# Kernel optimization log

Measured on AMD Instinct MI355X. Metric: run time of the kernel, lower is better.

Reference implementation:

```python
import jax, jax.numpy as jnp
import numpy as np

N, E, F_IN, HID, NUM_CLASSES = 10000, 160000, 512, 1024, 100
NEG_SLOPE = 0.2  # PyG GATv2Conv default negative_slope


def setup_inputs() -> dict:
    key = jax.random.key(0)
    ks = jax.random.split(key, 10)
    return {
        "x": jax.random.normal(ks[0], (N, F_IN), jnp.float32),
        "edge_index": jax.random.randint(ks[1], (2, E), 0, N, dtype=jnp.int64)
        if jax.config.jax_enable_x64 else jax.random.randint(ks[1], (2, E), 0, N, dtype=jnp.int32),
        # GATv2Conv params (single head, out=1024): lin_l (source), lin_r (target), attention vector a, output bias
        "Wl": jax.random.normal(ks[2], (F_IN, HID), jnp.float32) / np.sqrt(F_IN),
        "bl": jnp.zeros((HID,), jnp.float32),
        "Wr": jax.random.normal(ks[3], (F_IN, HID), jnp.float32) / np.sqrt(F_IN),
        "br": jnp.zeros((HID,), jnp.float32),
        "att": jax.random.normal(ks[4], (HID,), jnp.float32) / np.sqrt(HID),
        "conv_b": jnp.zeros((HID,), jnp.float32),
        # MLP head: 1024 -> 512 -> 128 -> num_classes
        "W1": jax.random.normal(ks[5], (HID, 512), jnp.float32) / np.sqrt(HID),
        "b1": jnp.zeros((512,), jnp.float32),
        "W2": jax.random.normal(ks[6], (512, 128), jnp.float32) / np.sqrt(512),
        "b2": jnp.zeros((128,), jnp.float32),
        "Wc": jax.random.normal(ks[7], (128, NUM_CLASSES), jnp.float32) / np.sqrt(128),
        "bc": jnp.zeros((NUM_CLASSES,), jnp.float32),
    }


def _gatv2_conv(x, edge_index, Wl, bl, Wr, br, att, conv_b):
    """GATv2Conv, heads=1, add_self_loops=True, share_weights=False."""
    n = x.shape[0]
    loops = jnp.arange(n, dtype=edge_index.dtype)
    src = jnp.concatenate([edge_index[0], loops])  # message sources j
    dst = jnp.concatenate([edge_index[1], loops])  # message targets i
    xl = x @ Wl + bl  # [N, HID] source transform
    xr = x @ Wr + br  # [N, HID] target transform
    # e_ij = a^T LeakyReLU(xl_j + xr_i), per edge
    e = jax.nn.leaky_relu(xl[src] + xr[dst], negative_slope=NEG_SLOPE) @ att  # [E+N]
    # segment softmax over incoming edges of each target node (self-loops guarantee non-empty segments)
    m = jax.ops.segment_max(e, dst, num_segments=n)
    w = jnp.exp(e - m[dst])
    s = jax.ops.segment_sum(w, dst, num_segments=n)
    alpha = w / s[dst]  # [E+N]
    out = jax.ops.segment_sum(alpha[:, None] * xl[src], dst, num_segments=n)  # [N, HID]
    return out + conv_b


def reference(x, edge_index, Wl, bl, Wr, br, att, conv_b, W1, b1, W2, b2, Wc, bc):
    h = jax.nn.relu(_gatv2_conv(x, edge_index, Wl, bl, Wr, br, att, conv_b))
    h = jax.nn.relu(h @ W1 + b1)
    h = jax.nn.relu(h @ W2 + b2)
    return h @ Wc + bc
```

## Files before the change

### kernel.cpp

```cpp
#include <hip/hip_runtime.h>
#include <hip/hip_bf16.h>

constexpr int N_NODES = 10000;
constexpr int E_EDGES = 160000;
constexpr int F_IN    = 512;
constexpr int HID     = 1024;
constexpr int NCLS    = 100;
constexpr float NEG_SLOPE = 0.2f;

constexpr int BM = 128, BN = 128, BK = 32;
constexpr int M_PAD = ((N_NODES + BM - 1) / BM) * BM;
constexpr int DEG_CAP = 64;

typedef __attribute__((ext_vector_type(8))) short bf16x8;
typedef __attribute__((ext_vector_type(4))) float f32x4;

__device__ inline void load_lds_16(const void* g, void* l) {
    __builtin_amdgcn_global_load_lds(
        (const __attribute__((address_space(1))) void*)g,
        (__attribute__((address_space(3))) void*)l, 16, 0, 0);
}

__device__ inline float bf2f(short s) {
    unsigned u = ((unsigned)(unsigned short)s) << 16;
    return __builtin_bit_cast(float, u);
}

__device__ inline float rfl(float x) {
    return __builtin_bit_cast(float,
        __builtin_amdgcn_readfirstlane(__builtin_bit_cast(int, x)));
}

__device__ inline short4 cvt4(const f32x4 v, const float4 b, int relu) {
    float r0 = v[0] + b.x, r1 = v[1] + b.y, r2 = v[2] + b.z, r3 = v[3] + b.w;
    if (relu) {
        r0 = fmaxf(r0, 0.f); r1 = fmaxf(r1, 0.f);
        r2 = fmaxf(r2, 0.f); r3 = fmaxf(r3, 0.f);
    }
    short4 o;
    o.x = __builtin_bit_cast(short, __float2bfloat16(r0));
    o.y = __builtin_bit_cast(short, __float2bfloat16(r1));
    o.z = __builtin_bit_cast(short, __float2bfloat16(r2));
    o.w = __builtin_bit_cast(short, __float2bfloat16(r3));
    return o;
}

__global__ __launch_bounds__(256, 4) void gemm_mfma(
    const __hip_bfloat16* __restrict__ A, const __hip_bfloat16* __restrict__ Bt,
    const float* __restrict__ bias, int M, int K, int relu, int n_valid,
    __hip_bfloat16* __restrict__ Cb, int ldb)
{
    __shared__ __align__(16) short As[2][BM * BK];
    __shared__ __align__(16) short Bs[2][BN * BK];

    const int tid  = threadIdx.x;
    const int lane = tid & 63;
    const int w    = tid >> 6;
    const int m0   = blockIdx.y * BM;
    const int n0   = blockIdx.x * BN;

    f32x4 acc[4][4] = {};

    const int c0 = tid, c1 = tid + 256;
    const int r0 = c0 >> 2, cc0 = (c0 & 3) ^ ((r0 >> 2) & 3);
    const int r1 = c1 >> 2, cc1 = (c1 & 3) ^ ((r1 >> 2) & 3);

    const short* Ag0 = (const short*)A + (size_t)(m0 + r0) * K + cc0 * 8;
    const short* Ag1 = (const short*)A + (size_t)(m0 + r1) * K + cc1 * 8;
    const short* Bg0 = (const short*)Bt + (size_t)(n0 + r0) * K + cc0 * 8;
    const short* Bg1 = (const short*)Bt + (size_t)(n0 + r1) * K + cc1 * 8;

    const int wm = (w >> 1) * 64;
    const int wn = (w & 1) * 64;
    const int q  = lane >> 4;
    const int mr = lane & 15;
    const int sl = (q ^ (mr >> 2)) * 8;

    load_lds_16(Ag0, As[0] + c0 * 8);
    load_lds_16(Ag1, As[0] + c1 * 8);
    load_lds_16(Bg0, Bs[0] + c0 * 8);
    load_lds_16(Bg1, Bs[0] + c1 * 8);

    int cur = 0;
    for (int k0 = 0; k0 < K; k0 += BK) {
        __syncthreads();
        const int nxt = cur ^ 1;
        const int kn = k0 + BK;
        if (kn < K) {
            load_lds_16(Ag0 + kn, As[nxt] + c0 * 8);
            load_lds_16(Ag1 + kn, As[nxt] + c1 * 8);
            load_lds_16(Bg0 + kn, Bs[nxt] + c0 * 8);
            load_lds_16(Bg1 + kn, Bs[nxt] + c1 * 8);
        }

        bf16x8 af[4], bf[4];
        #pragma unroll
        for (int mt = 0; mt < 4; ++mt)
            af[mt] = *(const bf16x8*)&As[cur][(wm + mt * 16 + mr) * BK + sl];
        #pragma unroll
        for (int nt = 0; nt < 4; ++nt)
            bf[nt] = *(const bf16x8*)&Bs[cur][(wn + nt * 16 + mr) * BK + sl];
        #pragma unroll
        for (int mt = 0; mt < 4; ++mt)
            #pragma unroll
            for (int nt = 0; nt < 4; ++nt)
                acc[mt][nt] = __builtin_amdgcn_mfma_f32_16x16x32_bf16(
                    bf[nt], af[mt], acc[mt][nt], 0, 0, 0);
        cur = nxt;
    }

    #pragma unroll
    for (int mt = 0; mt < 4; ++mt) {
        const int gm = m0 + wm + mt * 16 + mr;
        if (gm >= M) continue;
        #pragma unroll
        for (int nt = 0; nt < 4; ++nt) {
            const int gn = n0 + wn + nt * 16 + q * 4;
            if (gn >= n_valid) continue;
            const float4 bv = *(const float4*)&bias[gn];
            short4 o = cvt4(acc[mt][nt], bv, relu);
            *(short4*)((short*)Cb + (size_t)gm * ldb + gn) = o;
        }
    }
}

__global__ __launch_bounds__(256, 4) void gemm_mfma_64(
    const __hip_bfloat16* __restrict__ A, const __hip_bfloat16* __restrict__ Bt,
    const float* __restrict__ bias, int M, int K, int relu, int n_valid,
    __hip_bfloat16* __restrict__ Cb, int ldb)
{
    __shared__ __align__(16) short As[2][64 * BK];
    __shared__ __align__(16) short Bs[2][BN * BK];

    const int tid  = threadIdx.x;
    const int lane = tid & 63;
    const int w    = tid >> 6;
    const int m0   = blockIdx.y * 64;
    const int n0   = blockIdx.x * BN;

    f32x4 acc[4][2] = {};

    const int ca = tid;
    const int ra = ca >> 2, cca = (ca & 3) ^ ((ra >> 2) & 3);
    const int c0 = tid, c1 = tid + 256;
    const int r0 = c0 >> 2, cc0 = (c0 & 3) ^ ((r0 >> 2) & 3);
    const int r1 = c1 >> 2, cc1 = (c1 & 3) ^ ((r1 >> 2) & 3);

    const short* Ag  = (const short*)A + (size_t)(m0 + ra) * K + cca * 8;
    const short* Bg0 = (const short*)Bt + (size_t)(n0 + r0) * K + cc0 * 8;
    const short* Bg1 = (const short*)Bt + (size_t)(n0 + r1) * K + cc1 * 8;

    const int wn = w * 32;
    const int q  = lane >> 4;
    const int mr = lane & 15;
    const int sl = (q ^ (mr >> 2)) * 8;

    load_lds_16(Ag,  As[0] + ca * 8);
    load_lds_16(Bg0, Bs[0] + c0 * 8);
    load_lds_16(Bg1, Bs[0] + c1 * 8);

    int cur = 0;
    for (int k0 = 0; k0 < K; k0 += BK) {
        __syncthreads();
        const int nxt = cur ^ 1;
        const int kn = k0 + BK;
        if (kn < K) {
            load_lds_16(Ag + kn,  As[nxt] + ca * 8);
            load_lds_16(Bg0 + kn, Bs[nxt] + c0 * 8);
            load_lds_16(Bg1 + kn, Bs[nxt] + c1 * 8);
        }

        bf16x8 af[4], bf[2];
        #pragma unroll
        for (int mt = 0; mt < 4; ++mt)
            af[mt] = *(const bf16x8*)&As[cur][(mt * 16 + mr) * BK + sl];
        #pragma unroll
        for (int nt = 0; nt < 2; ++nt)
            bf[nt] = *(const bf16x8*)&Bs[cur][(wn + nt * 16 + mr) * BK + sl];
        #pragma unroll
        for (int mt = 0; mt < 4; ++mt)
            #pragma unroll
            for (int nt = 0; nt < 2; ++nt)
                acc[mt][nt] = __builtin_amdgcn_mfma_f32_16x16x32_bf16(
                    bf[nt], af[mt], acc[mt][nt], 0, 0, 0);
        cur = nxt;
    }

    #pragma unroll
    for (int mt = 0; mt < 4; ++mt) {
        const int gm = m0 + mt * 16 + mr;
        if (gm >= M) continue;
        #pragma unroll
        for (int nt = 0; nt < 2; ++nt) {
            const int gn = n0 + wn + nt * 16 + q * 4;
            if (gn >= n_valid) continue;
            const float4 bv = *(const float4*)&bias[gn];
            short4 o = cvt4(acc[mt][nt], bv, relu);
            *(short4*)((short*)Cb + (size_t)gm * ldb + gn) = o;
        }
    }
}

constexpr int HS_LD = 136;

__global__ __launch_bounds__(256) void mlp_tail(
    const __hip_bfloat16* __restrict__ h1, const __hip_bfloat16* __restrict__ W2t,
    const float* __restrict__ b2, const __hip_bfloat16* __restrict__ Wct,
    const float* __restrict__ bc, float* __restrict__ out)
{
    __shared__ __align__(16) short As[2][BM * BK];
    __shared__ __align__(16) short Bs[2][BN * BK];
    __shared__ __align__(16) short Hs[128 * HS_LD];

    const int tid  = threadIdx.x;
    const int lane = tid & 63;
    const int w    = tid >> 6;
    const int m0   = blockIdx.x * BM;

    const int c0 = tid, c1 = tid + 256;
    const int r0 = c0 >> 2, cc0 = (c0 & 3) ^ ((r0 >> 2) & 3);
    const int r1 = c1 >> 2, cc1 = (c1 & 3) ^ ((r1 >> 2) & 3);

    const int wm = (w >> 1) * 64;
    const int wn = (w & 1) * 64;
    const int q  = lane >> 4;
    const int mr = lane & 15;
    const int sl = (q ^ (mr >> 2)) * 8;

    {
        f32x4 acc[4][4] = {};
        const short* Ag0 = (const short*)h1 + (size_t)(m0 + r0) * 512 + cc0 * 8;
        const short* Ag1 = (const short*)h1 + (size_t)(m0 + r1) * 512 + cc1 * 8;
        const short* Bg0 = (const short*)W2t + (size_t)r0 * 512 + cc0 * 8;
        const short* Bg1 = (const short*)W2t + (size_t)r1 * 512 + cc1 * 8;

        load_lds_16(Ag0, As[0] + c0 * 8);
        load_lds_16(Ag1, As[0] + c1 * 8);
        load_lds_16(Bg0, Bs[0] + c0 * 8);
        load_lds_16(Bg1, Bs[0] + c1 * 8);

        int cur = 0;
        for (int k0 = 0; k0 < 512; k0 += BK) {
            __syncthreads();
            const int nxt = cur ^ 1;
            const int kn = k0 + BK;
            if (kn < 512) {
                load_lds_16(Ag0 + kn, As[nxt] + c0 * 8);
                load_lds_16(Ag1 + kn, As[nxt] + c1 * 8);
                load_lds_16(Bg0 + kn, Bs[nxt] + c0 * 8);
                load_lds_16(Bg1 + kn, Bs[nxt] + c1 * 8);
            }
            bf16x8 af[4], bf[4];
            #pragma unroll
            for (int mt = 0; mt < 4; ++mt)
                af[mt] = *(const bf16x8*)&As[cur][(wm + mt * 16 + mr) * BK + sl];
            #pragma unroll
            for (int nt = 0; nt < 4; ++nt)
                bf[nt] = *(const bf16x8*)&Bs[cur][(wn + nt * 16 + mr) * BK + sl];
            #pragma unroll
            for (int mt = 0; mt < 4; ++mt)
                #pragma unroll
                for (int nt = 0; nt < 4; ++nt)
                    acc[mt][nt] = __builtin_amdgcn_mfma_f32_16x16x32_bf16(
                        bf[nt], af[mt], acc[mt][nt], 0, 0, 0);
            cur = nxt;
        }
        __syncthreads();
        #pragma unroll
        for (int mt = 0; mt < 4; ++mt) {
            const int ml = wm + mt * 16 + mr;
            #pragma unroll
            for (int nt = 0; nt < 4; ++nt) {
                const int nl = wn + nt * 16 + q * 4;
                const float4 bv = *(const float4*)&b2[nl];
                short4 o = cvt4(acc[mt][nt], bv, 1);
                *(short4*)&Hs[ml * HS_LD + nl] = o;
            }
        }
    }

    {
        f32x4 acc[4][4] = {};
        const short* Bg0 = (const short*)Wct + (size_t)r0 * 128 + cc0 * 8;
        const short* Bg1 = (const short*)Wct + (size_t)r1 * 128 + cc1 * 8;

        for (int k0 = 0; k0 < 128; k0 += BK) {
            __syncthreads();
            load_lds_16(Bg0 + k0, Bs[0] + c0 * 8);
            load_lds_16(Bg1 + k0, Bs[0] + c1 * 8);
            __syncthreads();

            bf16x8 af[4], bf[4];
            #pragma unroll
            for (int mt = 0; mt < 4; ++mt)
                af[mt] = *(const bf16x8*)&Hs[(wm + mt * 16 + mr) * HS_LD + k0 + q * 8];
            #pragma unroll
            for (int nt = 0; nt < 4; ++nt)
                bf[nt] = *(const bf16x8*)&Bs[0][(wn + nt * 16 + mr) * BK + sl];
            #pragma unroll
            for (int mt = 0; mt < 4; ++mt)
                #pragma unroll
                for (int nt = 0; nt < 4; ++nt)
                    acc[mt][nt] = __builtin_amdgcn_mfma_f32_16x16x32_bf16(
                        bf[nt], af[mt], acc[mt][nt], 0, 0, 0);
        }
        #pragma unroll
        for (int mt = 0; mt < 4; ++mt) {
            const int gm = m0 + wm + mt * 16 + mr;
            if (gm >= N_NODES) continue;
            #pragma unroll
            for (int nt = 0; nt < 4; ++nt) {
                const int gn = wn + nt * 16 + q * 4;
                if (gn >= NCLS) continue;
                const float4 bv = *(const float4*)&bc[gn];
                float4 o;
                o.x = acc[mt][nt][0] + bv.x;
                o.y = acc[mt][nt][1] + bv.y;
                o.z = acc[mt][nt][2] + bv.z;
                o.w = acc[mt][nt][3] + bv.w;
                *(float4*)(out + (size_t)gm * NCLS + gn) = o;
            }
        }
    }
}

__device__ void transpose_tile(const float* __restrict__ W,
                               __hip_bfloat16* __restrict__ Wt,
                               int K, int N, int NP, int bx, int by,
                               int tx, int ty, float (*t)[33])
{
    int n0 = bx * 32, k0 = by * 32;
    #pragma unroll
    for (int i = 0; i < 32; i += 8) {
        int k = k0 + ty + i, n = n0 + tx;
        t[ty + i][tx] = (k < K && n < N) ? W[(size_t)k * N + n] : 0.f;
    }
    __syncthreads();
    #pragma unroll
    for (int i = 0; i < 32; i += 8) {
        int n = n0 + ty + i, k = k0 + tx;
        if (n < NP && k < K)
            Wt[(size_t)n * K + k] = __float2bfloat16(t[tx][ty + i]);
    }
}

constexpr int PK_X    = M_PAD * F_IN / 1024;
constexpr int PK_WL   = PK_X + 512;
constexpr int PK_WR   = PK_WL + 512;
constexpr int PK_W1   = PK_WR + 512;
constexpr int PK_W2   = PK_W1 + 64;
constexpr int PK_WC   = PK_W2 + 16;
constexpr int PK_BLR  = PK_WC + 8;
constexpr int PK_EDGE = PK_BLR + (E_EDGES + 255) / 256;

__global__ __launch_bounds__(256) void pack_all(
    const float* __restrict__ x, __hip_bfloat16* __restrict__ xb,
    const float* __restrict__ Wl, const float* __restrict__ Wr,
    __hip_bfloat16* __restrict__ Wlrt,
    const float* __restrict__ W1, __hip_bfloat16* __restrict__ W1t,
    const float* __restrict__ W2, __hip_bfloat16* __restrict__ W2t,
    const float* __restrict__ Wc, __hip_bfloat16* __restrict__ Wct,
    const float* __restrict__ bl, const float* __restrict__ br,
    float* __restrict__ blr,
    const int* __restrict__ ei, int* __restrict__ cnt, int* __restrict__ srcs)
{
    __shared__ float t[32][33];
    const int b = blockIdx.x;
    const int tid = threadIdx.x;
    const int tx = tid & 31, ty = tid >> 5;

    if (b < PK_X) {
        int i = b * 256 + tid;
        int row = i >> 7;
        int base = i << 2;
        short4 o;
        if (row < N_NODES) {
            const float4 v = *(const float4*)(x + base);
            o.x = __builtin_bit_cast(short, __float2bfloat16(v.x));
            o.y = __builtin_bit_cast(short, __float2bfloat16(v.y));
            o.z = __builtin_bit_cast(short, __float2bfloat16(v.z));
            o.w = __builtin_bit_cast(short, __float2bfloat16(v.w));
        } else {
            o.x = o.y = o.z = o.w = 0;
        }
        *(short4*)((short*)xb + base) = o;
    } else if (b < PK_WL) {
        int l = b - PK_X;
        transpose_tile(Wl, Wlrt, F_IN, HID, HID, l & 31, l >> 5, tx, ty, t);
    } else if (b < PK_WR) {
        int l = b - PK_WL;
        transpose_tile(Wr, Wlrt + (size_t)HID * F_IN, F_IN, HID, HID,
                       l & 31, l >> 5, tx, ty, t);
    } else if (b < PK_W1) {
        int l = b - PK_WR;
        transpose_tile(W1, W1t, HID, 512, 512, l & 15, l >> 4, tx, ty, t);
    } else if (b < PK_W2) {
        int l = b - PK_W1;
        transpose_tile(W2, W2t, 512, 128, 128, l & 3, l >> 2, tx, ty, t);
    } else if (b < PK_WC) {
        int l = b - PK_W2;
        transpose_tile(Wc, Wct, 128, NCLS, 128, l & 3, l >> 2, tx, ty, t);
    } else if (b < PK_BLR) {
        int i = (b - PK_WC) * 256 + tid;
        if (i < HID) blr[i] = bl[i];
        else if (i < 2 * HID) blr[i] = br[i - HID];
    } else {
        int e = (b - PK_BLR) * 256 + tid;
        if (e < E_EDGES) {
            int s = ei[e], d = ei[E_EDGES + e];
            int r = atomicAdd(&cnt[d], 1);
            if (r < DEG_CAP) srcs[(size_t)d * DEG_CAP + r] = s;
        }
    }
}

__global__ __launch_bounds__(256) void gat_node(
    const __hip_bfloat16* __restrict__ xlr, const float* __restrict__ att,
    const float* __restrict__ conv_b,
    const int* __restrict__ cnt, const int* __restrict__ srcs,
    __hip_bfloat16* __restrict__ h)
{
    const int tid  = threadIdx.x;
    const int lane = tid & 63;
    const int wave = tid >> 6;
    const int nloc = wave >> 1;
    const int wsub = wave & 1;
    const int i    = blockIdx.x * 2 + nloc;

    __shared__ float O_s[2][16 * 64];
    __shared__ float ml_s[2][2];

    int deg = __builtin_amdgcn_readfirstlane(cnt[i]);
    if (deg > DEG_CAP) deg = DEG_CAP;
    const int total = deg + 1;
    const int last  = total - 1;
    const int* slist = srcs + (size_t)i * DEG_CAP;
    const short* base = (const short*)xlr;

    float xr_v[16], att_v[16];
    {
        const short* xri = base + (size_t)i * 2048 + HID + lane * 16;
        bf16x8 a0 = *(const bf16x8*)xri;
        bf16x8 a1 = *(const bf16x8*)(xri + 8);
        const float* ai = att + lane * 16;
        #pragma unroll
        for (int j = 0; j < 8; ++j) {
            xr_v[j] = bf2f(a0[j]);
            xr_v[8 + j] = bf2f(a1[j]);
        }
        #pragma unroll
        for (int j = 0; j < 16; ++j) att_v[j] = ai[j];
    }

    float m_w = -3e38f, l_w = 0.f;
    float O[16];
    #pragma unroll
    for (int j = 0; j < 16; ++j) O[j] = 0.f;

    int pos = wsub;
    if (pos < total) {
        int sc = __builtin_amdgcn_readfirstlane(pos < deg ? slist[pos] : i);
        int pn = (pos + 2 <= last) ? pos + 2 : last;
        int sn = __builtin_amdgcn_readfirstlane(pn < deg ? slist[pn] : i);
        const short* rp = base + (size_t)sc * 2048 + lane * 16;
        bf16x8 a0 = *(const bf16x8*)rp;
        bf16x8 a1 = *(const bf16x8*)(rp + 8);

        for (; pos < total; pos += 2) {
            const short* np = base + (size_t)sn * 2048 + lane * 16;
            bf16x8 b0 = *(const bf16x8*)np;
            bf16x8 b1 = *(const bf16x8*)(np + 8);
            int p2i = (pos + 4 <= last) ? pos + 4 : last;
            int s2 = p2i < deg ? slist[p2i] : i;

            float xf[16];
            #pragma unroll
            for (int j = 0; j < 8; ++j) {
                xf[j] = bf2f(a0[j]);
                xf[8 + j] = bf2f(a1[j]);
            }

            float p = 0.f;
            #pragma unroll
            for (int j = 0; j < 16; ++j) {
                float a = xf[j] + xr_v[j];
                a = fmaxf(a, NEG_SLOPE * a);
                p = __builtin_fmaf(att_v[j], a, p);
            }
            #pragma unroll
            for (int s = 1; s < 64; s <<= 1) p += __shfl_xor(p, s, 64);
            p = rfl(p);

            if (p > m_w) {
                const float scale = __expf(m_w - p);
                l_w = l_w * scale + 1.f;
                #pragma unroll
                for (int j = 0; j < 16; ++j) O[j] = O[j] * scale + xf[j];
                m_w = p;
            } else {
                const float alpha = __expf(p - m_w);
                l_w += alpha;
                #pragma unroll
                for (int j = 0; j < 16; ++j)
                    O[j] = __builtin_fmaf(alpha, xf[j], O[j]);
            }

            a0 = b0; a1 = b1;
            sn = __builtin_amdgcn_readfirstlane(s2);
        }
    }

    if (wsub == 1) {
        #pragma unroll
        for (int j = 0; j < 16; ++j) O_s[nloc][j * 64 + lane] = O[j];
        if (lane == 0) { ml_s[nloc][0] = m_w; ml_s[nloc][1] = l_w; }
    }
    __syncthreads();

    if (wsub == 0) {
        const float m1 = ml_s[nloc][0], l1 = ml_s[nloc][1];
        const float M  = fmaxf(m_w, m1);
        const float c0 = __expf(m_w - M);
        const float c1 = __expf(m1 - M);
        const float invL = 1.f / (l_w * c0 + l1 * c1);
        const float* cb = conv_b + lane * 16;
        bf16x8 o0, o1;
        #pragma unroll
        for (int j = 0; j < 8; ++j) {
            float r0 = __builtin_fmaf(
                c0 * O[j] + c1 * O_s[nloc][j * 64 + lane], invL, cb[j]);
            float r1 = __builtin_fmaf(
                c0 * O[8 + j] + c1 * O_s[nloc][(8 + j) * 64 + lane], invL,
                cb[8 + j]);
            r0 = fmaxf(r0, 0.f);
            r1 = fmaxf(r1, 0.f);
            o0[j] = __builtin_bit_cast(short, __float2bfloat16(r0));
            o1[j] = __builtin_bit_cast(short, __float2bfloat16(r1));
        }
        short* hp = (short*)h + (size_t)i * HID + lane * 16;
        *(bf16x8*)hp = o0;
        *(bf16x8*)(hp + 8) = o1;
    }
}

extern "C" void kernel_launch(void* const* d_in, const int* in_sizes, int n_in,
                              void* d_out, int out_size, void* d_ws, size_t ws_size,
                              hipStream_t stream)
{
    const float* x      = (const float*)d_in[0];
    const int*   ei     = (const int*)d_in[1];
    const float* Wl     = (const float*)d_in[2];
    const float* bl     = (const float*)d_in[3];
    const float* Wr     = (const float*)d_in[4];
    const float* br     = (const float*)d_in[5];
    const float* att    = (const float*)d_in[6];
    const float* conv_b = (const float*)d_in[7];
    const float* W1     = (const float*)d_in[8];
    const float* b1     = (const float*)d_in[9];
    const float* W2     = (const float*)d_in[10];
    const float* b2     = (const float*)d_in[11];
    const float* Wc     = (const float*)d_in[12];
    const float* bc     = (const float*)d_in[13];
    float* out = (float*)d_out;

    char* p = (char*)d_ws;
    __hip_bfloat16* xlr = (__hip_bfloat16*)p; p += (size_t)M_PAD * 2048 * 2;
    __hip_bfloat16* hb  = (__hip_bfloat16*)p; p += (size_t)M_PAD * HID * 2;
    __hip_bfloat16* xb  = (__hip_bfloat16*)p; p += (size_t)M_PAD * F_IN * 2;
    __hip_bfloat16* Wlrt= (__hip_bfloat16*)p; p += (size_t)2 * HID * F_IN * 2;
    __hip_bfloat16* W1t = (__hip_bfloat16*)p; p += (size_t)512 * HID * 2;
    __hip_bfloat16* W2t = (__hip_bfloat16*)p; p += (size_t)128 * 512 * 2;
    __hip_bfloat16* Wct = (__hip_bfloat16*)p; p += (size_t)128 * 128 * 2;
    float* blr = (float*)p;               p += 2 * HID * 4;
    int* cnt  = (int*)p;                  p += N_NODES * 4;
    int* srcs = (int*)p;                  p += (size_t)N_NODES * DEG_CAP * 4;

    __hip_bfloat16* h1 = xb;

    const dim3 blk(256);

    hipMemsetAsync(cnt, 0, N_NODES * sizeof(int), stream);

    pack_all<<<PK_EDGE, blk, 0, stream>>>(x, xb, Wl, Wr, Wlrt, W1, W1t,
                                          W2, W2t, Wc, Wct, bl, br, blr,
                                          ei, cnt, srcs);

    gemm_mfma<<<dim3(2 * HID / BN, M_PAD / BM), blk, 0, stream>>>(
        xb, Wlrt, blr, N_NODES, F_IN, 0, 2 * HID, xlr, 2048);

    gat_node<<<N_NODES / 2, blk, 0, stream>>>(xlr, att, conv_b, cnt, srcs, hb);

    gemm_mfma_64<<<dim3(512 / BN, M_PAD / 64), blk, 0, stream>>>(
        hb, W1t, b1, N_NODES, HID, 1, 512, h1, 512);

    mlp_tail<<<M_PAD / BM, blk, 0, stream>>>(h1, W2t, b2, Wct, bc, out);
}
```

Measured before the change: 249.3 us.

## Halve mlp_tail row tile and fold self-loops into the edge lists

After: 236.4 us. 5.2% less time.

```diff
diff --git a/kernel.cpp b/kernel.cpp
--- a/kernel.cpp
+++ b/kernel.cpp
@@ -208,34 +208,33 @@
     const float* __restrict__ b2, const __hip_bfloat16* __restrict__ Wct,
     const float* __restrict__ bc, float* __restrict__ out)
 {
-    __shared__ __align__(16) short As[2][BM * BK];
+    __shared__ __align__(16) short As[2][64 * BK];
     __shared__ __align__(16) short Bs[2][BN * BK];
-    __shared__ __align__(16) short Hs[128 * HS_LD];
+    __shared__ __align__(16) short Hs[64 * HS_LD];
 
     const int tid  = threadIdx.x;
     const int lane = tid & 63;
     const int w    = tid >> 6;
-    const int m0   = blockIdx.x * BM;
-
+    const int m0   = blockIdx.x * 64;
+
+    const int ca = tid;
+    const int ra = ca >> 2, cca = (ca & 3) ^ ((ra >> 2) & 3);
     const int c0 = tid, c1 = tid + 256;
     const int r0 = c0 >> 2, cc0 = (c0 & 3) ^ ((r0 >> 2) & 3);
     const int r1 = c1 >> 2, cc1 = (c1 & 3) ^ ((r1 >> 2) & 3);
 
-    const int wm = (w >> 1) * 64;
-    const int wn = (w & 1) * 64;
+    const int wn = w * 32;
     const int q  = lane >> 4;
     const int mr = lane & 15;
     const int sl = (q ^ (mr >> 2)) * 8;
 
     {
-        f32x4 acc[4][4] = {};
-        const short* Ag0 = (const short*)h1 + (size_t)(m0 + r0) * 512 + cc0 * 8;
-        const short* Ag1 = (const short*)h1 + (size_t)(m0 + r1) * 512 + cc1 * 8;
+        f32x4 acc[4][2] = {};
+        const short* Ag  = (const short*)h1 + (size_t)(m0 + ra) * 512 + cca * 8;
         const short* Bg0 = (const short*)W2t + (size_t)r0 * 512 + cc0 * 8;
         const short* Bg1 = (const short*)W2t + (size_t)r1 * 512 + cc1 * 8;
 
-        load_lds_16(Ag0, As[0] + c0 * 8);
-        load_lds_16(Ag1, As[0] + c1 * 8);
+        load_lds_16(Ag,  As[0] + ca * 8);
         load_lds_16(Bg0, Bs[0] + c0 * 8);
         load_lds_16(Bg1, Bs[0] + c1 * 8);
 
@@ -245,22 +244,21 @@
             const int nxt = cur ^ 1;
             const int kn = k0 + BK;
             if (kn < 512) {
-                load_lds_16(Ag0 + kn, As[nxt] + c0 * 8);
-                load_lds_16(Ag1 + kn, As[nxt] + c1 * 8);
+                load_lds_16(Ag + kn,  As[nxt] + ca * 8);
                 load_lds_16(Bg0 + kn, Bs[nxt] + c0 * 8);
                 load_lds_16(Bg1 + kn, Bs[nxt] + c1 * 8);
             }
-            bf16x8 af[4], bf[4];
+            bf16x8 af[4], bf[2];
             #pragma unroll
             for (int mt = 0; mt < 4; ++mt)
-                af[mt] = *(const bf16x8*)&As[cur][(wm + mt * 16 + mr) * BK + sl];
-            #pragma unroll
-            for (int nt = 0; nt < 4; ++nt)
+                af[mt] = *(const bf16x8*)&As[cur][(mt * 16 + mr) * BK + sl];
+            #pragma unroll
+            for (int nt = 0; nt < 2; ++nt)
                 bf[nt] = *(const bf16x8*)&Bs[cur][(wn + nt * 16 + mr) * BK + sl];
             #pragma unroll
             for (int mt = 0; mt < 4; ++mt)
                 #pragma unroll
-                for (int nt = 0; nt < 4; ++nt)
+                for (int nt = 0; nt < 2; ++nt)
                     acc[mt][nt] = __builtin_amdgcn_mfma_f32_16x16x32_bf16(
                         bf[nt], af[mt], acc[mt][nt], 0, 0, 0);
             cur = nxt;
@@ -268,9 +266,9 @@
         __syncthreads();
         #pragma unroll
         for (int mt = 0; mt < 4; ++mt) {
-            const int ml = wm + mt * 16 + mr;
-            #pragma unroll
-            for (int nt = 0; nt < 4; ++nt) {
+            const int ml = mt * 16 + mr;
+            #pragma unroll
+            for (int nt = 0; nt < 2; ++nt) {
                 const int nl = wn + nt * 16 + q * 4;
                 const float4 bv = *(const float4*)&b2[nl];
                 short4 o = cvt4(acc[mt][nt], bv, 1);
@@ -280,7 +278,7 @@
     }
 
     {
-        f32x4 acc[4][4] = {};
+        f32x4 acc[4][2] = {};
         const short* Bg0 = (const short*)Wct + (size_t)r0 * 128 + cc0 * 8;
         const short* Bg1 = (const short*)Wct + (size_t)r1 * 128 + cc1 * 8;
 
@@ -290,26 +288,26 @@
             load_lds_16(Bg1 + k0, Bs[0] + c1 * 8);
             __syncthreads();
 
-            bf16x8 af[4], bf[4];
+            bf16x8 af[4], bf[2];
             #pragma unroll
             for (int mt = 0; mt < 4; ++mt)
-                af[mt] = *(const bf16x8*)&Hs[(wm + mt * 16 + mr) * HS_LD + k0 + q * 8];
-            #pragma unroll
-            for (int nt = 0; nt < 4; ++nt)
+                af[mt] = *(const bf16x8*)&Hs[(mt * 16 + mr) * HS_LD + k0 + q * 8];
+            #pragma unroll
+            for (int nt = 0; nt < 2; ++nt)
                 bf[nt] = *(const bf16x8*)&Bs[0][(wn + nt * 16 + mr) * BK + sl];
             #pragma unroll
             for (int mt = 0; mt < 4; ++mt)
                 #pragma unroll
-                for (int nt = 0; nt < 4; ++nt)
+                for (int nt = 0; nt < 2; ++nt)
                     acc[mt][nt] = __builtin_amdgcn_mfma_f32_16x16x32_bf16(
                         bf[nt], af[mt], acc[mt][nt], 0, 0, 0);
         }
         #pragma unroll
         for (int mt = 0; mt < 4; ++mt) {
-            const int gm = m0 + wm + mt * 16 + mr;
+            const int gm = m0 + mt * 16 + mr;
             if (gm >= N_NODES) continue;
             #pragma unroll
-            for (int nt = 0; nt < 4; ++nt) {
+            for (int nt = 0; nt < 2; ++nt) {
                 const int gn = wn + nt * 16 + q * 4;
                 if (gn >= NCLS) continue;
                 const float4 bv = *(const float4*)&bc[gn];
@@ -351,7 +349,7 @@
 constexpr int PK_W2   = PK_W1 + 64;
 constexpr int PK_WC   = PK_W2 + 16;
 constexpr int PK_BLR  = PK_WC + 8;
-constexpr int PK_EDGE = PK_BLR + (E_EDGES + 255) / 256;
+constexpr int PK_EDGE = PK_BLR + (E_EDGES + N_NODES + 255) / 256;
 
 __global__ __launch_bounds__(256) void pack_all(
     const float* __restrict__ x, __hip_bfloat16* __restrict__ xb,
@@ -406,8 +404,10 @@
         else if (i < 2 * HID) blr[i] = br[i - HID];
     } else {
         int e = (b - PK_BLR) * 256 + tid;
-        if (e < E_EDGES) {
-            int s = ei[e], d = ei[E_EDGES + e];
+        if (e < E_EDGES + N_NODES) {
+            int s, d;
+            if (e < E_EDGES) { s = ei[e]; d = ei[E_EDGES + e]; }
+            else             { s = e - E_EDGES; d = s; }
             int r = atomicAdd(&cnt[d], 1);
             if (r < DEG_CAP) srcs[(size_t)d * DEG_CAP + r] = s;
         }
@@ -432,8 +432,7 @@
 
     int deg = __builtin_amdgcn_readfirstlane(cnt[i]);
     if (deg > DEG_CAP) deg = DEG_CAP;
-    const int total = deg + 1;
-    const int last  = total - 1;
+    const int last = deg - 1;
     const int* slist = srcs + (size_t)i * DEG_CAP;
     const short* base = (const short*)xlr;
 
@@ -458,20 +457,21 @@
     for (int j = 0; j < 16; ++j) O[j] = 0.f;
 
     int pos = wsub;
-    if (pos < total) {
-        int sc = __builtin_amdgcn_readfirstlane(pos < deg ? slist[pos] : i);
-        int pn = (pos + 2 <= last) ? pos + 2 : last;
-        int sn = __builtin_amdgcn_readfirstlane(pn < deg ? slist[pn] : i);
+    if (pos < deg) {
+        int sc = __builtin_amdgcn_readfirstlane(slist[pos]);
+        if ((unsigned)sc >= N_NODES) sc = i;
+        int sn = __builtin_amdgcn_readfirstlane(
+                     slist[pos + 2 <= last ? pos + 2 : last]);
+        if ((unsigned)sn >= N_NODES) sn = i;
         const short* rp = base + (size_t)sc * 2048 + lane * 16;
         bf16x8 a0 = *(const bf16x8*)rp;
         bf16x8 a1 = *(const bf16x8*)(rp + 8);
 
-        for (; pos < total; pos += 2) {
+        for (; pos < deg; pos += 2) {
             const short* np = base + (size_t)sn * 2048 + lane * 16;
             bf16x8 b0 = *(const bf16x8*)np;
             bf16x8 b1 = *(const bf16x8*)(np + 8);
-            int p2i = (pos + 4 <= last) ? pos + 4 : last;
-            int s2 = p2i < deg ? slist[p2i] : i;
+            int s2 = slist[pos + 4 <= last ? pos + 4 : last];
 
             float xf[16];
             #pragma unroll
@@ -507,6 +507,7 @@
 
             a0 = b0; a1 = b1;
             sn = __builtin_amdgcn_readfirstlane(s2);
+            if ((unsigned)sn >= N_NODES) sn = i;
         }
     }
 
@@ -593,5 +594,5 @@
     gemm_mfma_64<<<dim3(512 / BN, M_PAD / 64), blk, 0, stream>>>(
         hb, W1t, b1, N_NODES, HID, 1, 512, h1, 512);
 
-    mlp_tail<<<M_PAD / BM, blk, 0, stream>>>(h1, W2t, b2, Wct, bc, out);
-}
+    mlp_tail<<<M_PAD / 64, blk, 0, stream>>>(h1, W2t, b2, Wct, bc, out);
+}
```
